# Performance work log

Hardware: AMD Instinct MI355X
Metric: run time of the kernel (lower is better)

## Reference

```python
import jax, jax.numpy as jnp
import numpy as np

TOP_K = 2
SCALING = 16.0 / 8.0  # alpha / rank


def setup_inputs() -> dict:
    key = jax.random.key(0)
    ks = jax.random.split(key, 9)
    B, V, D, P = 32, 21, 512, 64
    IN, OUT, E, R, H = D * P, 96, 8, 8, 256
    return {
        "x": jax.random.normal(ks[0], (B, V, D, P), jnp.float32),
        "W_base": jax.random.normal(ks[1], (OUT, IN), jnp.float32) * (IN ** -0.5),
        "b_base": jax.random.normal(ks[2], (OUT,), jnp.float32) * 0.01,
        "W1": jax.random.normal(ks[3], (H, D), jnp.float32) * (D ** -0.5),
        "b1": jax.random.normal(ks[4], (H,), jnp.float32) * 0.01,
        "W2": jax.random.normal(ks[5], (E, H), jnp.float32) * (H ** -0.5),
        "b2": jax.random.normal(ks[6], (E,), jnp.float32) * 0.01,
        "lora_A": jax.random.normal(ks[7], (E, R, IN), jnp.float32) * (IN ** -0.5),
        "lora_B": jax.random.normal(ks[8], (E, OUT, R), jnp.float32) * (R ** -0.5),
    }


def reference(x, W_base, b_base, W1, b1, W2, b2, lora_A, lora_B):
    B, V, D, P = x.shape
    E = lora_A.shape[0]
    # FlattenHead: flatten last two dims, then linear (dropout is identity in eval)
    flat = x.reshape(B, V, D * P)                      # [B, V, IN]
    base_out = flat @ W_base.T + b_base                # [B, V, OUT]
    # Router: pool over n_vars then patch dim -> [B, D]
    pooled = x.mean(axis=1).mean(axis=-1)
    h = jax.nn.relu(pooled @ W1.T + b1)
    logits = h @ W2.T + b2                             # [B, E]
    probs = jax.nn.softmax(logits, axis=-1)
    topw, topi = jax.lax.top_k(probs, TOP_K)           # [B, K]
    topw = topw / jnp.clip(topw.sum(-1, keepdims=True), 1e-6)
    # All LoRA experts (matches original dense compute), then weighted combine
    temp = jnp.einsum("bvi,eri->ebvr", flat, lora_A)   # [E, B, V, R]
    delta = jnp.einsum("ebvr,eor->ebvo", temp, lora_B) * SCALING  # [E, B, V, OUT]
    # Scatter top-k weights into dense [B, E] then combine (top-k sparse combine)
    w_full = jnp.zeros((B, E), x.dtype).at[jnp.arange(B)[:, None], topi].add(topw)
    moe_delta = jnp.einsum("be,ebvo->bvo", w_full, delta)
    return base_out + moe_delta, probs
```

## Files before the change

### kernel.cpp

```cpp
#include <hip/hip_runtime.h>

#define B_DIM 32
#define V_DIM 21
#define D_DIM 512
#define P_DIM 64
#define M_TOTAL 672
#define K_TOTAL 32768
#define OUT_DIM 96
#define E_DIM 8
#define R_DIM 8
#define H_DIM 256
#define N_TOTAL 160
#define SCALING 2.0f
#define POOL_SCALE (1.0f / (V_DIM * (float)P_DIM))

#define KSPLIT 64
#define K_PER_SPLIT (K_TOTAL / KSPLIT)
#define KSTEPS (K_PER_SPLIT / 32)
#define SMN (M_TOTAL * N_TOTAL)
#define RC_ROWS 2

typedef __attribute__((ext_vector_type(4))) float floatx4;
typedef __attribute__((ext_vector_type(8))) short short8;

__device__ __forceinline__ unsigned short f2bf(float f) {
  union { float f; unsigned int u; } v; v.f = f;
  unsigned int u = v.u + (0x7FFFu + ((v.u >> 16) & 1u));
  return (unsigned short)(u >> 16);
}

__global__ __launch_bounds__(256)
void convW_kernel(const float* __restrict__ W_base, const float* __restrict__ lora_A,
                  short* __restrict__ Wb, float* __restrict__ pooled) {
  int gid = blockIdx.x * 256 + threadIdx.x;
  if (blockIdx.x < 64) pooled[gid] = 0.0f;
  size_t base = (size_t)gid * 8;
  int row = (int)(base >> 15);
  int k = (int)(base & 32767);
  const float* src = (row < OUT_DIM) ? (W_base + ((size_t)row << 15) + k)
                                     : (lora_A + ((size_t)(row - OUT_DIM) << 15) + k);
  floatx4 v0 = ((const floatx4*)src)[0];
  floatx4 v1 = ((const floatx4*)src)[1];
  short8 sv;
  sv[0] = (short)f2bf(v0[0]); sv[1] = (short)f2bf(v0[1]);
  sv[2] = (short)f2bf(v0[2]); sv[3] = (short)f2bf(v0[3]);
  sv[4] = (short)f2bf(v1[0]); sv[5] = (short)f2bf(v1[1]);
  sv[6] = (short)f2bf(v1[2]); sv[7] = (short)f2bf(v1[3]);
  *(short8*)(Wb + base) = sv;
}

__global__ __launch_bounds__(256, 3)
void gemm_kernel(const float* __restrict__ x, const short* __restrict__ Wb,
                 float* __restrict__ P, float* __restrict__ pooled) {
  const int tid = threadIdx.x;
  const int wave = tid >> 6;
  const int lane = tid & 63;
  const int quad = lane >> 4;
  const int l16 = lane & 15;
  const int m0w = blockIdx.x * 64 + wave * 16;
  if (m0w >= M_TOTAL) return;
  const int ky = blockIdx.y;
  const int kbase = ky * K_PER_SPLIT;
  const int m = m0w + l16;
  const int bb = m / V_DIM;
  const float* xp = x + (size_t)m * K_TOTAL + kbase + quad * 8;
  const short* wp = Wb + (size_t)l16 * K_TOTAL + kbase + quad * 8;

  floatx4 acc[10];
  #pragma unroll
  for (int nt = 0; nt < 10; ++nt) acc[nt] = (floatx4)(0.0f);

  floatx4 a0 = ((const floatx4*)xp)[0];
  floatx4 a1 = *(const floatx4*)(xp + 4);
  float dsum = 0.0f;

  #pragma unroll
  for (int c = 0; c < KSTEPS; ++c) {
    floatx4 n0 = (floatx4)(0.0f), n1 = (floatx4)(0.0f);
    if (c + 1 < KSTEPS) {
      n0 = *(const floatx4*)(xp + (c + 1) * 32);
      n1 = *(const floatx4*)(xp + (c + 1) * 32 + 4);
    }
    short8 pb[10];
    #pragma unroll
    for (int nt = 0; nt < 10; ++nt)
      pb[nt] = *(const short8*)(wp + (size_t)nt * 16 * K_TOTAL + c * 32);
    short8 af;
    af[0] = (short)f2bf(a0[0]); af[1] = (short)f2bf(a0[1]);
    af[2] = (short)f2bf(a0[2]); af[3] = (short)f2bf(a0[3]);
    af[4] = (short)f2bf(a1[0]); af[5] = (short)f2bf(a1[1]);
    af[6] = (short)f2bf(a1[2]); af[7] = (short)f2bf(a1[3]);
    #pragma unroll
    for (int nt = 0; nt < 10; ++nt)
      acc[nt] = __builtin_amdgcn_mfma_f32_16x16x32_bf16(af, pb[nt], acc[nt], 0, 0, 0);
    float s8 = ((a0[0] + a0[1]) + (a0[2] + a0[3])) +
               ((a1[0] + a1[1]) + (a1[2] + a1[3]));
    s8 += __shfl_xor(s8, 16, 64);
    s8 += __shfl_xor(s8, 32, 64);
    if ((c & 1) == 0) {
      dsum = s8;
    } else if (quad == 0) {
      int d = (kbase >> 6) + (c >> 1);
      atomicAdd(&pooled[bb * D_DIM + d], (dsum + s8) * POOL_SCALE);
    }
    a0 = n0; a1 = n1;
  }

  float* Pp = P + (size_t)ky * SMN + (size_t)(m0w + quad * 4) * N_TOTAL + l16;
  #pragma unroll
  for (int r = 0; r < 4; ++r)
    #pragma unroll
    for (int nt = 0; nt < 10; ++nt)
      Pp[(size_t)r * N_TOTAL + nt * 16] = acc[nt][r];
}

__global__ __launch_bounds__(256)
void router_kernel(const float* __restrict__ pooled, const float* __restrict__ W1,
                   const float* __restrict__ b1, const float* __restrict__ W2,
                   const float* __restrict__ b2, float* __restrict__ wfull,
                   float* __restrict__ probs_out) {
  __shared__ float sp[D_DIM];
  __shared__ float sh[H_DIM];
  __shared__ float slog[E_DIM];
  const int b = blockIdx.x;
  const int t = threadIdx.x;
  sp[t] = pooled[b * D_DIM + t];
  sp[t + 256] = pooled[b * D_DIM + t + 256];
  __syncthreads();
  float acc = b1[t];
  const float* w1r = W1 + (size_t)t * D_DIM;
  for (int d = 0; d < D_DIM; ++d) acc += sp[d] * w1r[d];
  sh[t] = fmaxf(acc, 0.0f);
  __syncthreads();
  if (t < E_DIM) {
    float a = b2[t];
    const float* w2r = W2 + t * H_DIM;
    for (int j = 0; j < H_DIM; ++j) a += sh[j] * w2r[j];
    slog[t] = a;
  }
  __syncthreads();
  if (t == 0) {
    float p[E_DIM];
    float mx = slog[0];
    for (int e = 1; e < E_DIM; ++e) mx = fmaxf(mx, slog[e]);
    float se = 0.0f;
    for (int e = 0; e < E_DIM; ++e) { p[e] = __expf(slog[e] - mx); se += p[e]; }
    float inv = 1.0f / se;
    for (int e = 0; e < E_DIM; ++e) { p[e] *= inv; probs_out[b * E_DIM + e] = p[e]; }
    int i0 = 0;
    for (int e = 1; e < E_DIM; ++e) if (p[e] > p[i0]) i0 = e;
    int i1 = (i0 == 0) ? 1 : 0;
    for (int e = 0; e < E_DIM; ++e) if (e != i0 && p[e] > p[i1]) i1 = e;
    float s2 = p[i0] + p[i1];
    float invs = 1.0f / fmaxf(s2, 1e-6f);
    for (int e = 0; e < E_DIM; ++e) {
      float w = 0.0f;
      if (e == i0) w += p[i0] * invs;
      if (e == i1) w += p[i1] * invs;
      wfull[b * E_DIM + e] = w;
    }
  }
}

__global__ __launch_bounds__(256)
void reduce_combine_kernel(const float* __restrict__ P, const float* __restrict__ b_base,
                           const float* __restrict__ lora_B, const float* __restrict__ wfull,
                           float* __restrict__ out) {
  __shared__ float sS[RC_ROWS * N_TOTAL];
  const int t = threadIdx.x;
  const size_t base = (size_t)blockIdx.x * (RC_ROWS * N_TOTAL);
  for (int s = t; s < RC_ROWS * N_TOTAL; s += 256) {
    const float* Pp = P + base + s;
    float a = 0.0f;
    #pragma unroll 8
    for (int k = 0; k < KSPLIT; ++k) a += Pp[(size_t)k * SMN];
    sS[s] = a;
  }
  __syncthreads();
  if (t < RC_ROWS * OUT_DIM) {
    int mr = t / OUT_DIM;
    int o = t - mr * OUT_DIM;
    int mm = blockIdx.x * RC_ROWS + mr;
    int b = mm / V_DIM;
    const float* srow = sS + mr * N_TOTAL;
    float res = srow[o] + b_base[o];
    float moe = 0.0f;
    #pragma unroll
    for (int e = 0; e < E_DIM; ++e) {
      float we = wfull[b * E_DIM + e];
      if (we != 0.0f) {
        const float* lb = lora_B + ((size_t)e * OUT_DIM + o) * R_DIM;
        float dd = 0.0f;
        #pragma unroll
        for (int r = 0; r < R_DIM; ++r) dd += srow[OUT_DIM + e * R_DIM + r] * lb[r];
        moe += we * dd;
      }
    }
    out[(size_t)mm * OUT_DIM + o] = res + SCALING * moe;
  }
}

extern "C" void kernel_launch(void* const* d_in, const int* in_sizes, int n_in,
                              void* d_out, int out_size, void* d_ws, size_t ws_size,
                              hipStream_t stream) {
  const float* x      = (const float*)d_in[0];
  const float* W_base = (const float*)d_in[1];
  const float* b_base = (const float*)d_in[2];
  const float* W1     = (const float*)d_in[3];
  const float* b1     = (const float*)d_in[4];
  const float* W2     = (const float*)d_in[5];
  const float* b2     = (const float*)d_in[6];
  const float* lora_A = (const float*)d_in[7];
  const float* lora_B = (const float*)d_in[8];
  float* out = (float*)d_out;

  float* ws     = (float*)d_ws;
  float* pooled = ws;
  float* wfull  = ws + 16384;
  short* Wb     = (short*)(wfull + 256);
  float* P      = (float*)(Wb + (size_t)N_TOTAL * K_TOTAL);

  convW_kernel<<<(N_TOTAL * K_TOTAL / 8 + 255) / 256, 256, 0, stream>>>(
      W_base, lora_A, Wb, pooled);
  gemm_kernel<<<dim3(11, KSPLIT), 256, 0, stream>>>(x, Wb, P, pooled);
  router_kernel<<<B_DIM, 256, 0, stream>>>(pooled, W1, b1, W2, b2, wfull,
                                           out + (size_t)M_TOTAL * OUT_DIM);
  reduce_combine_kernel<<<M_TOTAL / RC_ROWS, 256, 0, stream>>>(
      P, b_base, lora_B, wfull, out);
}
```

Baseline: 251.6 us.

## Stage GEMM operands through LDS with register prefetch and block-local pooling

The GEMM kernel now loads 64x128 tiles of x and 160x128 tiles of the bf16 weights into shared memory with coalesced loads. Each chunk is held in registers, converted and written to LDS while the MFMAs consume the previous chunk. Previously each wave streamed its own rows and the full weight matrix directly from global memory. The split-K factor is halved to 32 and the pooled-sum atomics are first accumulated in shared memory, then flushed once per block. This cuts redundant weight traffic across waves and global atomics, at the cost of more LDS use, extra barriers and lower occupancy (launch bound 2).

```diff
diff --git a/kernel.cpp b/kernel.cpp
--- a/kernel.cpp
+++ b/kernel.cpp
@@ -14,14 +14,18 @@
 #define SCALING 2.0f
 #define POOL_SCALE (1.0f / (V_DIM * (float)P_DIM))
 
-#define KSPLIT 64
+#define BM 64
+#define BK 128
+#define KSPLIT 32
 #define K_PER_SPLIT (K_TOTAL / KSPLIT)
-#define KSTEPS (K_PER_SPLIT / 32)
+#define CHUNKS (K_PER_SPLIT / BK)
+#define LDS_K (BK + 8)
 #define SMN (M_TOTAL * N_TOTAL)
 #define RC_ROWS 2
 
 typedef __attribute__((ext_vector_type(4))) float floatx4;
 typedef __attribute__((ext_vector_type(8))) short short8;
+typedef __attribute__((ext_vector_type(4))) short shortx4;
 
 __device__ __forceinline__ unsigned short f2bf(float f) {
   union { float f; unsigned int u; } v; v.f = f;
@@ -49,69 +53,126 @@
   *(short8*)(Wb + base) = sv;
 }
 
-__global__ __launch_bounds__(256, 3)
+__global__ __launch_bounds__(256, 2)
 void gemm_kernel(const float* __restrict__ x, const short* __restrict__ Wb,
                  float* __restrict__ P, float* __restrict__ pooled) {
+  __shared__ short ldsA[BM * LDS_K];
+  __shared__ short ldsB[N_TOTAL * LDS_K];
+  __shared__ float lds_pool[5 * 16];
   const int tid = threadIdx.x;
+  const int m0 = blockIdx.x * BM;
+  const int ky = blockIdx.y;
+  const int kbase = ky * K_PER_SPLIT;
+  const int lane = tid & 63;
   const int wave = tid >> 6;
-  const int lane = tid & 63;
   const int quad = lane >> 4;
   const int l16 = lane & 15;
-  const int m0w = blockIdx.x * 64 + wave * 16;
-  if (m0w >= M_TOTAL) return;
-  const int ky = blockIdx.y;
-  const int kbase = ky * K_PER_SPLIT;
-  const int m = m0w + l16;
-  const int bb = m / V_DIM;
-  const float* xp = x + (size_t)m * K_TOTAL + kbase + quad * 8;
-  const short* wp = Wb + (size_t)l16 * K_TOTAL + kbase + quad * 8;
+  const int b_first = m0 / V_DIM;
+  const int d_first = kbase >> 6;
+
+  if (tid < 80) lds_pool[tid] = 0.0f;
 
   floatx4 acc[10];
   #pragma unroll
   for (int nt = 0; nt < 10; ++nt) acc[nt] = (floatx4)(0.0f);
 
-  floatx4 a0 = ((const floatx4*)xp)[0];
-  floatx4 a1 = *(const floatx4*)(xp + 4);
-  float dsum = 0.0f;
-
-  #pragma unroll
-  for (int c = 0; c < KSTEPS; ++c) {
-    floatx4 n0 = (floatx4)(0.0f), n1 = (floatx4)(0.0f);
-    if (c + 1 < KSTEPS) {
-      n0 = *(const floatx4*)(xp + (c + 1) * 32);
-      n1 = *(const floatx4*)(xp + (c + 1) * 32 + 4);
+  floatx4 pa[8];
+  short8 pb[10];
+
+#define ISSUE(c)                                                                \
+  {                                                                             \
+    const int kc = kbase + (c) * BK;                                            \
+    _Pragma("unroll")                                                           \
+    for (int it = 0; it < 8; ++it) {                                            \
+      int idx = it * 256 + tid;                                                 \
+      int arow = idx >> 5;                                                      \
+      int u = idx & 31;                                                         \
+      int m = m0 + arow;                                                        \
+      pa[it] = (m < M_TOTAL)                                                    \
+          ? *(const floatx4*)(x + (size_t)m * K_TOTAL + kc + u * 4)             \
+          : (floatx4)(0.0f);                                                    \
+    }                                                                           \
+    _Pragma("unroll")                                                           \
+    for (int it = 0; it < 10; ++it) {                                           \
+      int idx = it * 256 + tid;                                                 \
+      int brow = idx >> 4;                                                      \
+      int g = idx & 15;                                                         \
+      pb[it] = *(const short8*)(Wb + (size_t)brow * K_TOTAL + kc + g * 8);      \
+    }                                                                           \
+  }
+
+#define CONVERT_WRITE(c)                                                        \
+  {                                                                             \
+    _Pragma("unroll")                                                           \
+    for (int it = 0; it < 8; ++it) {                                            \
+      int idx = it * 256 + tid;                                                 \
+      int arow = idx >> 5;                                                      \
+      int u = idx & 31;                                                         \
+      int m = m0 + arow;                                                        \
+      floatx4 v = pa[it];                                                       \
+        \
+      float s = (v[0] + v[1]) + (v[2] + v[3]);                                  \
+      s += __shfl_down(s, 8, 16);                                               \
+      s += __shfl_down(s, 4, 16);                                               \
+      s += __shfl_down(s, 2, 16);                                               \
+      s += __shfl_down(s, 1, 16);                                               \
+      if ((tid & 15) == 0 && m < M_TOTAL) {                                     \
+        int b_local = (m / V_DIM) - b_first;                                    \
+        int d_local = (c) * 2 + (u >> 4);                                       \
+        atomicAdd(&lds_pool[b_local * 16 + d_local], s);                        \
+      }                                                                         \
+      shortx4 sv;                                                               \
+      sv[0] = (short)f2bf(v[0]); sv[1] = (short)f2bf(v[1]);                     \
+      sv[2] = (short)f2bf(v[2]); sv[3] = (short)f2bf(v[3]);                     \
+      *(shortx4*)&ldsA[arow * LDS_K + u * 4] = sv;                              \
+    }                                                                           \
+    _Pragma("unroll")                                                           \
+    for (int it = 0; it < 10; ++it) {                                           \
+      int idx = it * 256 + tid;                                                 \
+      int brow = idx >> 4;                                                      \
+      int g = idx & 15;                                                         \
+      *(short8*)&ldsB[brow * LDS_K + g * 8] = pb[it];                           \
+    }                                                                           \
+  }
+
+  ISSUE(0);
+  __syncthreads();
+  CONVERT_WRITE(0);
+
+  for (int c = 0; c < CHUNKS; ++c) {
+    __syncthreads();
+    if (c + 1 < CHUNKS) ISSUE(c + 1);
+    #pragma unroll
+    for (int ks = 0; ks < 4; ++ks) {
+      const int ko = ks * 32 + quad * 8;
+      short8 a = *(const short8*)&ldsA[(wave * 16 + l16) * LDS_K + ko];
+      #pragma unroll
+      for (int nt = 0; nt < 10; ++nt) {
+        short8 b = *(const short8*)&ldsB[(nt * 16 + l16) * LDS_K + ko];
+        acc[nt] = __builtin_amdgcn_mfma_f32_16x16x32_bf16(a, b, acc[nt], 0, 0, 0);
+      }
     }
-    short8 pb[10];
+    __syncthreads();
+    if (c + 1 < CHUNKS) CONVERT_WRITE(c + 1);
+  }
+
+  {
+    const int mrow = m0 + wave * 16 + quad * 4;
+    float* Pp = P + (size_t)ky * SMN + (size_t)mrow * N_TOTAL + l16;
     #pragma unroll
-    for (int nt = 0; nt < 10; ++nt)
-      pb[nt] = *(const short8*)(wp + (size_t)nt * 16 * K_TOTAL + c * 32);
-    short8 af;
-    af[0] = (short)f2bf(a0[0]); af[1] = (short)f2bf(a0[1]);
-    af[2] = (short)f2bf(a0[2]); af[3] = (short)f2bf(a0[3]);
-    af[4] = (short)f2bf(a1[0]); af[5] = (short)f2bf(a1[1]);
-    af[6] = (short)f2bf(a1[2]); af[7] = (short)f2bf(a1[3]);
-    #pragma unroll
-    for (int nt = 0; nt < 10; ++nt)
-      acc[nt] = __builtin_amdgcn_mfma_f32_16x16x32_bf16(af, pb[nt], acc[nt], 0, 0, 0);
-    float s8 = ((a0[0] + a0[1]) + (a0[2] + a0[3])) +
-               ((a1[0] + a1[1]) + (a1[2] + a1[3]));
-    s8 += __shfl_xor(s8, 16, 64);
-    s8 += __shfl_xor(s8, 32, 64);
-    if ((c & 1) == 0) {
-      dsum = s8;
-    } else if (quad == 0) {
-      int d = (kbase >> 6) + (c >> 1);
-      atomicAdd(&pooled[bb * D_DIM + d], (dsum + s8) * POOL_SCALE);
-    }
-    a0 = n0; a1 = n1;
-  }
-
-  float* Pp = P + (size_t)ky * SMN + (size_t)(m0w + quad * 4) * N_TOTAL + l16;
-  #pragma unroll
-  for (int r = 0; r < 4; ++r)
-    #pragma unroll
-    for (int nt = 0; nt < 10; ++nt)
-      Pp[(size_t)r * N_TOTAL + nt * 16] = acc[nt][r];
+    for (int r = 0; r < 4; ++r)
+      if (mrow + r < M_TOTAL)
+        #pragma unroll
+        for (int nt = 0; nt < 10; ++nt)
+          Pp[(size_t)r * N_TOTAL + nt * 16] = acc[nt][r];
+  }
+
+  if (tid < 80) {
+    int b = b_first + (tid >> 4);
+    int d = d_first + (tid & 15);
+    if (b < B_DIM)
+      atomicAdd(&pooled[b * D_DIM + d], lds_pool[tid] * POOL_SCALE);
+  }
 }
 
 __global__ __launch_bounds__(256)
```

After: 207.0 us. 1.22x faster.
